# Kernel tuning notes

Measured on AMD Instinct MI355X. Metric: run time of the kernel, lower is better.

The kernel has to match this reference:

```python
import jax, jax.numpy as jnp
import numpy as np

DEPTH = 3
MAX_NB = 10
HIDDEN = 128


def setup_inputs() -> dict:
    key = jax.random.key(0)
    k = jax.random.split(key, 14)
    B, A, E, H, NB = 64, 1024, 2048, HIDDEN, MAX_NB
    s = 0.05
    return {
        "input_atom": jax.random.normal(k[0], (B, A, 82), jnp.float32),
        "input_bond": jax.random.normal(k[1], (B, E, 6), jnp.float32),
        "atom_graph": jax.random.randint(k[2], (B, A, NB), 0, A),
        "bond_graph": jax.random.randint(k[3], (B, A, NB), 0, E),
        "num_nbs": jax.random.randint(k[4], (B, A), 0, NB + 1),
        "node_mask": jnp.ones((B, A), jnp.float32),
        "W_atom": jax.random.normal(k[5], (82, H), jnp.float32) * s,
        "W_nei_atom": jax.random.normal(k[6], (H, H), jnp.float32) * s,
        "W_nei_bond": jax.random.normal(k[7], (6, H), jnp.float32) * s,
        "W_self": jax.random.normal(k[8], (H, H), jnp.float32) * s,
        "W_U2": jax.random.normal(k[9], (H + 6, H), jnp.float32) * s,
        "b_U2": jax.random.normal(k[10], (H,), jnp.float32) * s,
        "W_U1": jax.random.normal(k[11], (2 * H, H), jnp.float32) * s,
        "b_U1": jax.random.normal(k[12], (H,), jnp.float32) * s,
    }


def reference(input_atom, input_bond, atom_graph, bond_graph, num_nbs, node_mask,
              W_atom, W_nei_atom, W_nei_bond, W_self, W_U2, b_U2, W_U1, b_U1):
    B, A, NB = atom_graph.shape
    H = W_atom.shape[1]
    atom_features = input_atom @ W_atom                       # [B, A, H]
    # neighbor validity mask: [B, A, NB, 1]
    mask_nei = (jnp.arange(NB)[None, None, :] < num_nbs[:, :, None]).astype(jnp.float32)[..., None]
    idx_a = atom_graph.reshape(B, A * NB, 1)
    idx_b = bond_graph.reshape(B, A * NB, 1)
    # bond neighbor features are loop-invariant: gather once
    fbond_nei = jnp.take_along_axis(input_bond, idx_b, axis=1).reshape(B, A, NB, 6)
    h_nei_bond = fbond_nei @ W_nei_bond                       # [B, A, NB, H]
    node_m = node_mask[..., None]                             # [B, A, 1]
    kernel = None
    for _ in range(DEPTH):
        fatom_nei = jnp.take_along_axis(atom_features, idx_a, axis=1).reshape(B, A, NB, H)
        h_nei = (fatom_nei @ W_nei_atom) * h_nei_bond         # [B, A, NB, H]
        f_nei = jnp.sum(h_nei * mask_nei, axis=2)             # [B, A, H]
        f_self = atom_features @ W_self                        # [B, A, H]
        kernel = f_nei * f_self * node_m
        l_nei = jnp.concatenate([fatom_nei, fbond_nei], axis=3)  # [B, A, NB, H+6]
        pre_label = l_nei @ W_U2 + b_U2
        nei_label = jnp.sum(pre_label * mask_nei, axis=2)      # [B, A, H]
        new_label = jnp.concatenate([atom_features, nei_label], axis=2)
        atom_features = new_label @ W_U1 + b_U1
    return kernel, atom_features
```

## Files before the change

kernel.cpp:

```cpp
#include <hip/hip_runtime.h>

constexpr int NB = 10, H = 128;
constexpr int M = 64 * 1024;
constexpr long SL = (long)M * H;

typedef __attribute__((ext_vector_type(8))) short s16x8;
typedef __attribute__((ext_vector_type(4))) float f32x4;

__device__ __forceinline__ ushort f2b(float f) {
    union { float f; uint u; } v; v.f = f;
    uint u = v.u;
    uint r = u + 0x7fffu + ((u >> 16) & 1u);
    return (ushort)(r >> 16);
}
__device__ __forceinline__ float b2f(ushort u) {
    union { uint u; float f; } v; v.u = ((uint)u) << 16; return v.f;
}

__device__ __forceinline__ int swz(int bid, int cpx) {
    return (bid & 7) * cpx + (bid >> 3);
}

template<int NC, int FLAGS>
__device__ __forceinline__ void gemm_body(
    int tg, const ushort* __restrict__ Abf, const ushort* __restrict__ WT,
    const ushort* __restrict__ FNb, const float* __restrict__ nmask,
    float* __restrict__ Cf, ushort* __restrict__ Cb)
{
    constexpr bool KOUT = FLAGS & 8, OF32 = FLAGS & 16;
    constexpr int K = NC * 32;
    const int lane = threadIdx.x & 63, wid = threadIdx.x >> 6;
    const int l15 = lane & 15, g = lane >> 4;

    s16x8 w[2][NC];
    #pragma unroll
    for (int ct = 0; ct < 2; ++ct)
        #pragma unroll
        for (int kc = 0; kc < NC; ++kc)
            w[ct][kc] = *(const s16x8*)(WT + (size_t)((2 * wid + ct) * 16 + l15) * K + kc * 32 + g * 8);

    #pragma unroll
    for (int i = 0; i < 4; ++i) {
        const int m0 = (tg * 4 + i) * 16;
        s16x8 ac[NC];
        #pragma unroll
        for (int kc = 0; kc < NC; ++kc)
            ac[kc] = *(const s16x8*)(Abf + (size_t)(m0 + l15) * K + kc * 32 + g * 8);

        f32x4 acc[2];
        #pragma unroll
        for (int ct = 0; ct < 2; ++ct) acc[ct] = (f32x4){0.f, 0.f, 0.f, 0.f};
        #pragma unroll
        for (int kc = 0; kc < NC; ++kc)
            #pragma unroll
            for (int ct = 0; ct < 2; ++ct)
                acc[ct] = __builtin_amdgcn_mfma_f32_16x16x32_bf16(ac[kc], w[ct][kc], acc[ct], 0, 0, 0);

        #pragma unroll
        for (int ct = 0; ct < 2; ++ct) {
            const int col = (2 * wid + ct) * 16 + l15;
            #pragma unroll
            for (int r = 0; r < 4; ++r) {
                const int m = m0 + 4 * g + r;
                const size_t o = (size_t)m * H + col;
                float v = acc[ct][r];
                if constexpr (KOUT) v = v * b2f(FNb[o]) * nmask[m];
                if constexpr (OF32) Cf[o] = v; else Cb[o] = f2b(v);
            }
        }
    }
}

template<bool OF32>
__device__ __forceinline__ void u1f_body(
    int tg, const ushort* __restrict__ AF, const ushort* __restrict__ SATOM,
    const ushort* __restrict__ FBSb, const ushort* __restrict__ WT,
    float* __restrict__ Cf, ushort* __restrict__ Cb)
{
    const int lane = threadIdx.x & 63, wid = threadIdx.x >> 6;
    const int l15 = lane & 15, g = lane >> 4;

    s16x8 w[2][9];
    #pragma unroll
    for (int ct = 0; ct < 2; ++ct)
        #pragma unroll
        for (int kc = 0; kc < 9; ++kc)
            w[ct][kc] = *(const s16x8*)(WT + (size_t)((2 * wid + ct) * 16 + l15) * 288 + kc * 32 + g * 8);

    #pragma unroll
    for (int i = 0; i < 4; ++i) {
        const int m0 = (tg * 4 + i) * 16;
        const size_t rb = (size_t)(m0 + l15) * H + g * 8;
        s16x8 ac[9];
        #pragma unroll
        for (int kc = 0; kc < 4; ++kc) {
            ac[kc]     = *(const s16x8*)(AF    + rb + kc * 32);
            ac[kc + 4] = *(const s16x8*)(SATOM + rb + kc * 32);
        }
        ac[8] = (s16x8){0,0,0,0,0,0,0,0};
        if (g == 0) ac[8] = *(const s16x8*)(FBSb + (size_t)(m0 + l15) * 8);

        f32x4 acc[2];
        #pragma unroll
        for (int ct = 0; ct < 2; ++ct) acc[ct] = (f32x4){0.f, 0.f, 0.f, 0.f};
        #pragma unroll
        for (int kc = 0; kc < 9; ++kc)
            #pragma unroll
            for (int ct = 0; ct < 2; ++ct)
                acc[ct] = __builtin_amdgcn_mfma_f32_16x16x32_bf16(ac[kc], w[ct][kc], acc[ct], 0, 0, 0);

        #pragma unroll
        for (int ct = 0; ct < 2; ++ct) {
            const int col = (2 * wid + ct) * 16 + l15;
            #pragma unroll
            for (int r = 0; r < 4; ++r) {
                const size_t o = (size_t)(m0 + 4 * g + r) * H + col;
                if constexpr (OF32) Cf[o] = acc[ct][r]; else Cb[o] = f2b(acc[ct][r]);
            }
        }
    }
}

template<int NC, int FLAGS>
__global__ __launch_bounds__(256, 4) void gemm_af(
    const ushort* __restrict__ Abf, const ushort* __restrict__ WT,
    const ushort* __restrict__ FNb, const float* __restrict__ nmask,
    float* __restrict__ Cf, ushort* __restrict__ Cb)
{
    gemm_body<NC, FLAGS>(swz(blockIdx.x, 128), Abf, WT, FNb, nmask, Cf, Cb);
}

template<bool OF32>
__global__ __launch_bounds__(256, 4) void u1f(
    const ushort* __restrict__ AF, const ushort* __restrict__ SATOM,
    const ushort* __restrict__ FBSb, const ushort* __restrict__ WT,
    float* __restrict__ Cf, ushort* __restrict__ Cb)
{
    u1f_body<OF32>(swz(blockIdx.x, 128), AF, SATOM, FBSb, WT, Cf, Cb);
}

__global__ __launch_bounds__(256, 4) void final2(
    const ushort* __restrict__ AF, const ushort* __restrict__ SATl,
    const ushort* __restrict__ FBSb, const ushort* __restrict__ WTu1f,
    const ushort* __restrict__ WTslf, const ushort* __restrict__ FNEIb,
    const float* __restrict__ nmask, float* __restrict__ out1,
    float* __restrict__ out0)
{
    if (blockIdx.x < 1024)
        u1f_body<true>(swz(blockIdx.x, 128), AF, SATl, FBSb, WTu1f, out1, nullptr);
    else
        gemm_body<4, 8 | 16>(swz(blockIdx.x - 1024, 128), AF, WTslf, FNEIb,
                             nmask, out0, nullptr);
}

__global__ __launch_bounds__(256, 8) void gather_satom(
    const ushort* __restrict__ AF, const int* __restrict__ ag,
    const int* __restrict__ nn, ushort* __restrict__ SATOM)
{
    const int bid = swz(blockIdx.x, 512);
    const int m  = bid * 16 + (threadIdx.x >> 4);
    const int c8 = (threadIdx.x & 15) * 8;
    const int b  = m >> 10;
    const int nnb = nn[m];
    const ushort* AFb = AF + ((size_t)b << 10) * H + c8;
    const int* agm = ag + (size_t)m * NB;

    int2 iv0 = *(const int2*)(agm + 0);
    int2 iv1 = *(const int2*)(agm + 2);
    int2 iv2 = *(const int2*)(agm + 4);
    int2 iv3 = *(const int2*)(agm + 6);
    int2 iv4 = *(const int2*)(agm + 8);

    float sacc[8];
    #pragma unroll
    for (int i = 0; i < 8; ++i) sacc[i] = 0.f;

    #define GS_STEP(nb, ia)                                              \
    if ((nb) < nnb) {                                                    \
        s16x8 av = *(const s16x8*)(AFb + (size_t)(ia) * H);              \
        _Pragma("unroll")                                                \
        for (int i = 0; i < 8; ++i) sacc[i] += b2f((ushort)av[i]);       \
    }
    GS_STEP(0, iv0.x) GS_STEP(1, iv0.y)
    GS_STEP(2, iv1.x) GS_STEP(3, iv1.y)
    GS_STEP(4, iv2.x) GS_STEP(5, iv2.y)
    GS_STEP(6, iv3.x) GS_STEP(7, iv3.y)
    GS_STEP(8, iv4.x) GS_STEP(9, iv4.y)
    #undef GS_STEP

    s16x8 so;
    #pragma unroll
    for (int i = 0; i < 8; ++i) so[i] = (short)f2b(sacc[i]);
    *(s16x8*)(SATOM + (size_t)m * H + c8) = so;
}

__global__ __launch_bounds__(256, 4) void gather_last(
    const ushort* __restrict__ AF, const ushort* __restrict__ ATW,
    const ushort* __restrict__ HB, const int* __restrict__ ag,
    const int* __restrict__ bg, const int* __restrict__ nn,
    ushort* __restrict__ SATOM, ushort* __restrict__ FNEIb)
{
    const int bid = swz(blockIdx.x, 512);
    const int m  = bid * 16 + (threadIdx.x >> 4);
    const int c8 = (threadIdx.x & 15) * 8;
    const int b  = m >> 10;
    const int nnb = nn[m];
    const ushort* AFb  = AF  + ((size_t)b << 10) * H + c8;
    const ushort* ATWb = ATW + ((size_t)b << 10) * H + c8;
    const ushort* HBb  = HB  + ((size_t)b << 11) * H + c8;
    const int* agm = ag + (size_t)m * NB;
    const int* bgm = bg + (size_t)m * NB;

    int2 ia0 = *(const int2*)(agm + 0), ib0 = *(const int2*)(bgm + 0);
    int2 ia1 = *(const int2*)(agm + 2), ib1 = *(const int2*)(bgm + 2);
    int2 ia2 = *(const int2*)(agm + 4), ib2 = *(const int2*)(bgm + 4);
    int2 ia3 = *(const int2*)(agm + 6), ib3 = *(const int2*)(bgm + 6);
    int2 ia4 = *(const int2*)(agm + 8), ib4 = *(const int2*)(bgm + 8);

    float sacc[8], facc[8];
    #pragma unroll
    for (int i = 0; i < 8; ++i) { sacc[i] = 0.f; facc[i] = 0.f; }

    #define GL_STEP(nb, ia, ib)                                          \
    if ((nb) < nnb) {                                                    \
        s16x8 av = *(const s16x8*)(AFb  + (size_t)(ia) * H);             \
        s16x8 tv = *(const s16x8*)(ATWb + (size_t)(ia) * H);             \
        s16x8 hv = *(const s16x8*)(HBb  + (size_t)(ib) * H);             \
        _Pragma("unroll")                                                \
        for (int i = 0; i < 8; ++i) {                                    \
            sacc[i] += b2f((ushort)av[i]);                               \
            facc[i] += b2f((ushort)tv[i]) * b2f((ushort)hv[i]);          \
        }                                                                \
    }
    GL_STEP(0, ia0.x, ib0.x) GL_STEP(1, ia0.y, ib0.y)
    GL_STEP(2, ia1.x, ib1.x) GL_STEP(3, ia1.y, ib1.y)
    GL_STEP(4, ia2.x, ib2.x) GL_STEP(5, ia2.y, ib2.y)
    GL_STEP(6, ia3.x, ib3.x) GL_STEP(7, ia3.y, ib3.y)
    GL_STEP(8, ia4.x, ib4.x) GL_STEP(9, ia4.y, ib4.y)
    #undef GL_STEP

    s16x8 so, fo;
    #pragma unroll
    for (int i = 0; i < 8; ++i) { so[i] = (short)f2b(sacc[i]); fo[i] = (short)f2b(facc[i]); }
    *(s16x8*)(SATOM + (size_t)m * H + c8) = so;
    *(s16x8*)(FNEIb + (size_t)m * H + c8) = fo;
}

__global__ __launch_bounds__(256) void prep_all(
    const float* __restrict__ Wa, const float* __restrict__ Wna,
    const float* __restrict__ Ws, const float* __restrict__ Wu2,
    const float* __restrict__ bu2, const float* __restrict__ Wu1,
    const float* __restrict__ bu1, const float* __restrict__ bond,
    const int* __restrict__ bg, const int* __restrict__ nn,
    const float* __restrict__ ia, const float* __restrict__ Wnb,
    ushort* __restrict__ WTs, ushort* __restrict__ FBSb,
    ushort* __restrict__ AFin, ushort* __restrict__ HB)
{
    const int bid = blockIdx.x;
    if (bid < 320) {
        int t = bid * 256 + threadIdx.x;
        const int tid = t;
        if (t < 128 * 96) { int n = t / 96, k = t % 96;
            WTs[tid] = (k < 82) ? f2b(Wa[k * H + n]) : 0; return; }
        t -= 128 * 96;
        if (t < 128 * 128) { int n = t / 128, k = t % 128;
            WTs[tid] = f2b(Wna[k * H + n]); return; }
        t -= 128 * 128;
        if (t < 128 * 128) { int n = t / 128, k = t % 128;
            WTs[tid] = f2b(Ws[k * H + n]); return; }
        t -= 128 * 128;
        {
            const int n = t / 288, k = t % 288;
            float v = 0.f;
            if (k < 128) {
                v = Wu1[k * H + n];
            } else if (k < 256) {
                const int kk = k - 128;
                float s = 0.f;
                for (int j = 0; j < 128; ++j) s += Wu2[kk * H + j] * Wu1[(128 + j) * H + n];
                v = s;
            } else {
                const int j = k - 256;
                if (j < 6) {
                    float s = 0.f;
                    for (int q = 0; q < 128; ++q) s += Wu2[(128 + j) * H + q] * Wu1[(128 + q) * H + n];
                    v = s;
                } else if (j == 6) {
                    float s = 0.f;
                    for (int q = 0; q < 128; ++q) s += bu2[q] * Wu1[(128 + q) * H + n];
                    v = s;
                } else if (j == 7) {
                    v = bu1[n];
                }
            }
            WTs[tid] = f2b(v);
            return;
        }
    } else if (bid < 576) {
        const int m = (bid - 320) * 256 + threadIdx.x;
        const int b = m >> 10;
        const int nnb = nn[m];
        float s[6] = {0,0,0,0,0,0};
        for (int nb = 0; nb < nnb; ++nb) {
            const int ib = bg[m * NB + nb];
            const float* fb = bond + ((size_t)(b << 11) + (size_t)ib) * 6;
            #pragma unroll
            for (int j = 0; j < 6; ++j) s[j] += fb[j];
        }
        s16x8 o;
        #pragma unroll
        for (int j = 0; j < 6; ++j) o[j] = (short)f2b(s[j]);
        o[6] = (short)f2b((float)nnb);
        o[7] = (short)f2b(1.0f);
        *(s16x8*)(FBSb + (size_t)m * 8) = o;
    } else if (bid < 3648) {
        const int tid = (bid - 576) * 256 + threadIdx.x;
        const int m = tid / 12, c = (tid % 12) * 8;
        s16x8 v;
        #pragma unroll
        for (int i = 0; i < 8; ++i) {
            const int k = c + i;
            v[i] = (short)(k < 82 ? f2b(ia[(size_t)m * 82 + k]) : 0);
        }
        *(s16x8*)(AFin + (size_t)m * 96 + c) = v;
    } else {
        const int t = (bid - 3648) * 256 + threadIdx.x;
        const int r = t >> 4, c8 = (t & 15) * 8;
        const float* fb = bond + (size_t)r * 6;
        const float2 f01 = *(const float2*)fb;
        const float2 f23 = *(const float2*)(fb + 2);
        const float2 f45 = *(const float2*)(fb + 4);
        s16x8 o;
        #pragma unroll
        for (int i = 0; i < 8; ++i) {
            const int c = c8 + i;
            const float v = f01.x * Wnb[0 * H + c] + f01.y * Wnb[1 * H + c]
                          + f23.x * Wnb[2 * H + c] + f23.y * Wnb[3 * H + c]
                          + f45.x * Wnb[4 * H + c] + f45.y * Wnb[5 * H + c];
            o[i] = (short)f2b(v);
        }
        *(s16x8*)(HB + (size_t)r * H + c8) = o;
    }
}

extern "C" void kernel_launch(void* const* d_in, const int* in_sizes, int n_in,
                              void* d_out, int out_size, void* d_ws, size_t ws_size,
                              hipStream_t stream)
{
    (void)in_sizes; (void)n_in; (void)out_size; (void)ws_size;

    const float* input_atom = (const float*)d_in[0];
    const float* input_bond = (const float*)d_in[1];
    const int*   atom_graph = (const int*)d_in[2];
    const int*   bond_graph = (const int*)d_in[3];
    const int*   num_nbs    = (const int*)d_in[4];
    const float* node_mask  = (const float*)d_in[5];
    const float* W_atom     = (const float*)d_in[6];
    const float* W_nei_atom = (const float*)d_in[7];
    const float* W_nei_bond = (const float*)d_in[8];
    const float* W_self     = (const float*)d_in[9];
    const float* W_U2       = (const float*)d_in[10];
    const float* b_U2       = (const float*)d_in[11];
    const float* W_U1       = (const float*)d_in[12];
    const float* b_U1       = (const float*)d_in[13];

    char* ws = (char*)d_ws;
    const size_t MB = 1024 * 1024;
    ushort* AF0   = (ushort*)(ws);
    ushort* AF1   = (ushort*)(ws + 16 * MB);
    ushort* SATw  = (ushort*)(ws + 32 * MB);
    ushort* ATW   = SATw;
    ushort* AFin  = (ushort*)(ws + 48 * MB);
    ushort* HB    = (ushort*)(ws + 64 * MB);
    ushort* SATl  = (ushort*)(ws + 96 * MB);
    ushort* FBSb  = (ushort*)(ws + 112 * MB);
    ushort* WTs_  = (ushort*)(ws + 113 * MB);

    ushort* WTa   = WTs_;
    ushort* WTna  = WTa   + 128 * 96;
    ushort* WTslf = WTna  + 128 * 128;
    ushort* WTu1f = WTslf + 128 * 128;

    float*  out0  = (float*)d_out;
    float*  out1  = out0 + SL;
    ushort* FNEIb = AF1;

    prep_all<<<11840, 256, 0, stream>>>(W_atom, W_nei_atom, W_self, W_U2, b_U2,
                                        W_U1, b_U1, input_bond, bond_graph,
                                        num_nbs, input_atom, W_nei_bond,
                                        WTs_, FBSb, AFin, HB);

    gemm_af<3, 0><<<1024, 256, 0, stream>>>(AFin, WTa, nullptr, nullptr,
                                            nullptr, AF0);

    gather_satom<<<4096, 256, 0, stream>>>(AF0, atom_graph, num_nbs, SATw);
    u1f<false><<<1024, 256, 0, stream>>>(AF0, SATw, FBSb, WTu1f, nullptr, AF1);
    gather_satom<<<4096, 256, 0, stream>>>(AF1, atom_graph, num_nbs, SATw);
    u1f<false><<<1024, 256, 0, stream>>>(AF1, SATw, FBSb, WTu1f, nullptr, AF0);

    gemm_af<4, 0><<<1024, 256, 0, stream>>>(AF0, WTna, nullptr, nullptr,
                                            nullptr, ATW);
    gather_last<<<4096, 256, 0, stream>>>(AF0, ATW, HB, atom_graph, bond_graph,
                                          num_nbs, SATl, FNEIb);
    final2<<<2048, 256, 0, stream>>>(AF0, SATl, FBSb, WTu1f, WTslf, FNEIb,
                                     node_mask, out1, out0);
}
```

Before: 193.3 us.

## Fuse neighbor-sum gather into U1 GEMM and move bond projection off prep

The neighbor-feature sum is now computed per wave directly in registers and fed straight into the U1 MFMA GEMM, removing the separate gather_satom kernels and the SATOM round trip through memory. Each wave now owns 16 rows across all 128 output columns and reloads weights from global/L2 per MFMA instead of keeping them in registers. The bond-hidden projection HB moves from prep_all into the ATW GEMM launch so it can overlap with it, and gather_last no longer sums atom features. The cost is heavier per-wave register use and repeated weight loads, with fewer waves working on each gather.

```diff
diff --git a/kernel.cpp b/kernel.cpp
--- a/kernel.cpp
+++ b/kernel.cpp
@@ -72,140 +72,158 @@
 }
 
 template<bool OF32>
-__device__ __forceinline__ void u1f_body(
-    int tg, const ushort* __restrict__ AF, const ushort* __restrict__ SATOM,
-    const ushort* __restrict__ FBSb, const ushort* __restrict__ WT,
-    float* __restrict__ Cf, ushort* __restrict__ Cb)
-{
-    const int lane = threadIdx.x & 63, wid = threadIdx.x >> 6;
+__device__ __forceinline__ void gu1_body(
+    int t, const ushort* __restrict__ AF, const ushort* __restrict__ FBSb,
+    const ushort* __restrict__ WT, const int* __restrict__ ag,
+    const int* __restrict__ nn, float* __restrict__ Cf, ushort* __restrict__ Cb)
+{
+    const int lane = threadIdx.x & 63;
     const int l15 = lane & 15, g = lane >> 4;
-
-    s16x8 w[2][9];
-    #pragma unroll
-    for (int ct = 0; ct < 2; ++ct)
-        #pragma unroll
-        for (int kc = 0; kc < 9; ++kc)
-            w[ct][kc] = *(const s16x8*)(WT + (size_t)((2 * wid + ct) * 16 + l15) * 288 + kc * 32 + g * 8);
-
-    #pragma unroll
-    for (int i = 0; i < 4; ++i) {
-        const int m0 = (tg * 4 + i) * 16;
-        const size_t rb = (size_t)(m0 + l15) * H + g * 8;
-        s16x8 ac[9];
-        #pragma unroll
-        for (int kc = 0; kc < 4; ++kc) {
-            ac[kc]     = *(const s16x8*)(AF    + rb + kc * 32);
-            ac[kc + 4] = *(const s16x8*)(SATOM + rb + kc * 32);
-        }
-        ac[8] = (s16x8){0,0,0,0,0,0,0,0};
-        if (g == 0) ac[8] = *(const s16x8*)(FBSb + (size_t)(m0 + l15) * 8);
-
-        f32x4 acc[2];
-        #pragma unroll
-        for (int ct = 0; ct < 2; ++ct) acc[ct] = (f32x4){0.f, 0.f, 0.f, 0.f};
-        #pragma unroll
-        for (int kc = 0; kc < 9; ++kc)
-            #pragma unroll
-            for (int ct = 0; ct < 2; ++ct)
-                acc[ct] = __builtin_amdgcn_mfma_f32_16x16x32_bf16(ac[kc], w[ct][kc], acc[ct], 0, 0, 0);
-
-        #pragma unroll
-        for (int ct = 0; ct < 2; ++ct) {
-            const int col = (2 * wid + ct) * 16 + l15;
-            #pragma unroll
-            for (int r = 0; r < 4; ++r) {
-                const size_t o = (size_t)(m0 + 4 * g + r) * H + col;
-                if constexpr (OF32) Cf[o] = acc[ct][r]; else Cb[o] = f2b(acc[ct][r]);
-            }
-        }
-    }
-}
-
-template<int NC, int FLAGS>
-__global__ __launch_bounds__(256, 4) void gemm_af(
+    const int m0 = t * 16;
+    const int row = m0 + l15;
+    const int b = row >> 10;
+    const ushort* AFb = AF + ((size_t)b << 10) * H + g * 8;
+    const int* agm = ag + (size_t)row * NB;
+    const int nnb = nn[row];
+
+    int2 iv0 = *(const int2*)(agm + 0);
+    int2 iv1 = *(const int2*)(agm + 2);
+    int2 iv2 = *(const int2*)(agm + 4);
+    int2 iv3 = *(const int2*)(agm + 6);
+    int2 iv4 = *(const int2*)(agm + 8);
+
+    float sacc[4][8];
+    #pragma unroll
+    for (int kc = 0; kc < 4; ++kc)
+        #pragma unroll
+        for (int i = 0; i < 8; ++i) sacc[kc][i] = 0.f;
+
+    #define GU_STEP(nb, ia)                                               \
+    if ((nb) < nnb) {                                                     \
+        const ushort* src = AFb + (size_t)(ia) * H;                       \
+        _Pragma("unroll")                                                 \
+        for (int kc = 0; kc < 4; ++kc) {                                  \
+            s16x8 v = *(const s16x8*)(src + kc * 32);                     \
+            _Pragma("unroll")                                             \
+            for (int i = 0; i < 8; ++i) sacc[kc][i] += b2f((ushort)v[i]); \
+        }                                                                 \
+    }
+    GU_STEP(0, iv0.x) GU_STEP(1, iv0.y)
+    GU_STEP(2, iv1.x) GU_STEP(3, iv1.y)
+    GU_STEP(4, iv2.x) GU_STEP(5, iv2.y)
+    GU_STEP(6, iv3.x) GU_STEP(7, iv3.y)
+    GU_STEP(8, iv4.x) GU_STEP(9, iv4.y)
+    #undef GU_STEP
+
+    s16x8 pa[4];
+    #pragma unroll
+    for (int kc = 0; kc < 4; ++kc)
+        #pragma unroll
+        for (int i = 0; i < 8; ++i) pa[kc][i] = (short)f2b(sacc[kc][i]);
+
+    s16x8 af[4];
+    const size_t rb = (size_t)row * H + g * 8;
+    #pragma unroll
+    for (int kc = 0; kc < 4; ++kc)
+        af[kc] = *(const s16x8*)(AF + rb + kc * 32);
+    s16x8 fb8 = (s16x8){0,0,0,0,0,0,0,0};
+    if (g == 0) fb8 = *(const s16x8*)(FBSb + (size_t)row * 8);
+
+    f32x4 acc[8];
+    #pragma unroll
+    for (int c = 0; c < 8; ++c) acc[c] = (f32x4){0.f, 0.f, 0.f, 0.f};
+
+    #pragma unroll
+    for (int kc = 0; kc < 9; ++kc) {
+        const s16x8 a = (kc < 4) ? af[kc] : ((kc < 8) ? pa[kc - 4] : fb8);
+        #pragma unroll
+        for (int c = 0; c < 8; ++c) {
+            s16x8 w = *(const s16x8*)(WT + (size_t)(c * 16 + l15) * 288 + kc * 32 + g * 8);
+            acc[c] = __builtin_amdgcn_mfma_f32_16x16x32_bf16(a, w, acc[c], 0, 0, 0);
+        }
+    }
+
+    #pragma unroll
+    for (int c = 0; c < 8; ++c) {
+        const int col = c * 16 + l15;
+        #pragma unroll
+        for (int r = 0; r < 4; ++r) {
+            const size_t o = (size_t)(m0 + 4 * g + r) * H + col;
+            if constexpr (OF32) Cf[o] = acc[c][r]; else Cb[o] = f2b(acc[c][r]);
+        }
+    }
+}
+
+__global__ __launch_bounds__(256, 4) void fused_gu1(
+    const ushort* __restrict__ AF, const ushort* __restrict__ FBSb,
+    const ushort* __restrict__ WT, const int* __restrict__ ag,
+    const int* __restrict__ nn, ushort* __restrict__ Cb)
+{
+    const int t = swz(blockIdx.x, 128) * 4 + (threadIdx.x >> 6);
+    gu1_body<false>(t, AF, FBSb, WT, ag, nn, nullptr, Cb);
+}
+
+__global__ __launch_bounds__(256, 4) void gemm_af3(
     const ushort* __restrict__ Abf, const ushort* __restrict__ WT,
-    const ushort* __restrict__ FNb, const float* __restrict__ nmask,
-    float* __restrict__ Cf, ushort* __restrict__ Cb)
-{
-    gemm_body<NC, FLAGS>(swz(blockIdx.x, 128), Abf, WT, FNb, nmask, Cf, Cb);
-}
-
-template<bool OF32>
-__global__ __launch_bounds__(256, 4) void u1f(
-    const ushort* __restrict__ AF, const ushort* __restrict__ SATOM,
-    const ushort* __restrict__ FBSb, const ushort* __restrict__ WT,
-    float* __restrict__ Cf, ushort* __restrict__ Cb)
-{
-    u1f_body<OF32>(swz(blockIdx.x, 128), AF, SATOM, FBSb, WT, Cf, Cb);
+    ushort* __restrict__ Cb)
+{
+    gemm_body<3, 0>(swz(blockIdx.x, 128), Abf, WT, nullptr, nullptr, nullptr, Cb);
+}
+
+__global__ __launch_bounds__(256, 4) void gemm_atw_hb(
+    const ushort* __restrict__ AF, const ushort* __restrict__ WTna,
+    const float* __restrict__ bond, const float* __restrict__ Wnb,
+    ushort* __restrict__ ATW, ushort* __restrict__ HB)
+{
+    if (blockIdx.x < 1024) {
+        gemm_body<4, 0>(swz(blockIdx.x, 128), AF, WTna, nullptr, nullptr,
+                        nullptr, ATW);
+    } else {
+        const int t = (blockIdx.x - 1024) * 256 + threadIdx.x;
+        const int r = t >> 4, c8 = (t & 15) * 8;
+        const float* fb = bond + (size_t)r * 6;
+        const float2 f01 = *(const float2*)fb;
+        const float2 f23 = *(const float2*)(fb + 2);
+        const float2 f45 = *(const float2*)(fb + 4);
+        s16x8 o;
+        #pragma unroll
+        for (int i = 0; i < 8; ++i) {
+            const int c = c8 + i;
+            const float v = f01.x * Wnb[0 * H + c] + f01.y * Wnb[1 * H + c]
+                          + f23.x * Wnb[2 * H + c] + f23.y * Wnb[3 * H + c]
+                          + f45.x * Wnb[4 * H + c] + f45.y * Wnb[5 * H + c];
+            o[i] = (short)f2b(v);
+        }
+        *(s16x8*)(HB + (size_t)r * H + c8) = o;
+    }
 }
 
 __global__ __launch_bounds__(256, 4) void final2(
-    const ushort* __restrict__ AF, const ushort* __restrict__ SATl,
-    const ushort* __restrict__ FBSb, const ushort* __restrict__ WTu1f,
-    const ushort* __restrict__ WTslf, const ushort* __restrict__ FNEIb,
-    const float* __restrict__ nmask, float* __restrict__ out1,
-    float* __restrict__ out0)
-{
-    if (blockIdx.x < 1024)
-        u1f_body<true>(swz(blockIdx.x, 128), AF, SATl, FBSb, WTu1f, out1, nullptr);
-    else
+    const ushort* __restrict__ AF, const ushort* __restrict__ FBSb,
+    const ushort* __restrict__ WTu1f, const ushort* __restrict__ WTslf,
+    const ushort* __restrict__ FNEIb, const int* __restrict__ ag,
+    const int* __restrict__ nn, const float* __restrict__ nmask,
+    float* __restrict__ out1, float* __restrict__ out0)
+{
+    if (blockIdx.x < 1024) {
+        const int t = swz(blockIdx.x, 128) * 4 + (threadIdx.x >> 6);
+        gu1_body<true>(t, AF, FBSb, WTu1f, ag, nn, out1, nullptr);
+    } else {
         gemm_body<4, 8 | 16>(swz(blockIdx.x - 1024, 128), AF, WTslf, FNEIb,
                              nmask, out0, nullptr);
-}
-
-__global__ __launch_bounds__(256, 8) void gather_satom(
-    const ushort* __restrict__ AF, const int* __restrict__ ag,
-    const int* __restrict__ nn, ushort* __restrict__ SATOM)
+    }
+}
+
+__global__ __launch_bounds__(256, 8) void gather_fnei(
+    const ushort* __restrict__ ATW, const ushort* __restrict__ HB,
+    const int* __restrict__ ag, const int* __restrict__ bg,
+    const int* __restrict__ nn, ushort* __restrict__ FNEIb)
 {
     const int bid = swz(blockIdx.x, 512);
     const int m  = bid * 16 + (threadIdx.x >> 4);
     const int c8 = (threadIdx.x & 15) * 8;
     const int b  = m >> 10;
     const int nnb = nn[m];
-    const ushort* AFb = AF + ((size_t)b << 10) * H + c8;
-    const int* agm = ag + (size_t)m * NB;
-
-    int2 iv0 = *(const int2*)(agm + 0);
-    int2 iv1 = *(const int2*)(agm + 2);
-    int2 iv2 = *(const int2*)(agm + 4);
-    int2 iv3 = *(const int2*)(agm + 6);
-    int2 iv4 = *(const int2*)(agm + 8);
-
-    float sacc[8];
-    #pragma unroll
-    for (int i = 0; i < 8; ++i) sacc[i] = 0.f;
-
-    #define GS_STEP(nb, ia)                                              \
-    if ((nb) < nnb) {                                                    \
-        s16x8 av = *(const s16x8*)(AFb + (size_t)(ia) * H);              \
-        _Pragma("unroll")                                                \
-        for (int i = 0; i < 8; ++i) sacc[i] += b2f((ushort)av[i]);       \
-    }
-    GS_STEP(0, iv0.x) GS_STEP(1, iv0.y)
-    GS_STEP(2, iv1.x) GS_STEP(3, iv1.y)
-    GS_STEP(4, iv2.x) GS_STEP(5, iv2.y)
-    GS_STEP(6, iv3.x) GS_STEP(7, iv3.y)
-    GS_STEP(8, iv4.x) GS_STEP(9, iv4.y)
-    #undef GS_STEP
-
-    s16x8 so;
-    #pragma unroll
-    for (int i = 0; i < 8; ++i) so[i] = (short)f2b(sacc[i]);
-    *(s16x8*)(SATOM + (size_t)m * H + c8) = so;
-}
-
-__global__ __launch_bounds__(256, 4) void gather_last(
-    const ushort* __restrict__ AF, const ushort* __restrict__ ATW,
-    const ushort* __restrict__ HB, const int* __restrict__ ag,
-    const int* __restrict__ bg, const int* __restrict__ nn,
-    ushort* __restrict__ SATOM, ushort* __restrict__ FNEIb)
-{
-    const int bid = swz(blockIdx.x, 512);
-    const int m  = bid * 16 + (threadIdx.x >> 4);
-    const int c8 = (threadIdx.x & 15) * 8;
-    const int b  = m >> 10;
-    const int nnb = nn[m];
-    const ushort* AFb  = AF  + ((size_t)b << 10) * H + c8;
     const ushort* ATWb = ATW + ((size_t)b << 10) * H + c8;
     const ushort* HBb  = HB  + ((size_t)b << 11) * H + c8;
     const int* agm = ag + (size_t)m * NB;
@@ -217,32 +235,28 @@
     int2 ia3 = *(const int2*)(agm + 6), ib3 = *(const int2*)(bgm + 6);
     int2 ia4 = *(const int2*)(agm + 8), ib4 = *(const int2*)(bgm + 8);
 
-    float sacc[8], facc[8];
-    #pragma unroll
-    for (int i = 0; i < 8; ++i) { sacc[i] = 0.f; facc[i] = 0.f; }
-
-    #define GL_STEP(nb, ia, ib)                                          \
-    if ((nb) < nnb) {                                                    \
-        s16x8 av = *(const s16x8*)(AFb  + (size_t)(ia) * H);             \
-        s16x8 tv = *(const s16x8*)(ATWb + (size_t)(ia) * H);             \
-        s16x8 hv = *(const s16x8*)(HBb  + (size_t)(ib) * H);             \
-        _Pragma("unroll")                                                \
-        for (int i = 0; i < 8; ++i) {                                    \
-            sacc[i] += b2f((ushort)av[i]);                               \
-            facc[i] += b2f((ushort)tv[i]) * b2f((ushort)hv[i]);          \
-        }                                                                \
-    }
-    GL_STEP(0, ia0.x, ib0.x) GL_STEP(1, ia0.y, ib0.y)
-    GL_STEP(2, ia1.x, ib1.x) GL_STEP(3, ia1.y, ib1.y)
-    GL_STEP(4, ia2.x, ib2.x) GL_STEP(5, ia2.y, ib2.y)
-    GL_STEP(6, ia3.x, ib3.x) GL_STEP(7, ia3.y, ib3.y)
-    GL_STEP(8, ia4.x, ib4.x) GL_STEP(9, ia4.y, ib4.y)
-    #undef GL_STEP
-
-    s16x8 so, fo;
-    #pragma unroll
-    for (int i = 0; i < 8; ++i) { so[i] = (short)f2b(sacc[i]); fo[i] = (short)f2b(facc[i]); }
-    *(s16x8*)(SATOM + (size_t)m * H + c8) = so;
+    float facc[8];
+    #pragma unroll
+    for (int i = 0; i < 8; ++i) facc[i] = 0.f;
+
+    #define GF_STEP(nb, ia, ib)                                           \
+    if ((nb) < nnb) {                                                     \
+        s16x8 tv = *(const s16x8*)(ATWb + (size_t)(ia) * H);              \
+        s16x8 hv = *(const s16x8*)(HBb  + (size_t)(ib) * H);              \
+        _Pragma("unroll")                                                 \
+        for (int i = 0; i < 8; ++i)                                       \
+            facc[i] += b2f((ushort)tv[i]) * b2f((ushort)hv[i]);           \
+    }
+    GF_STEP(0, ia0.x, ib0.x) GF_STEP(1, ia0.y, ib0.y)
+    GF_STEP(2, ia1.x, ib1.x) GF_STEP(3, ia1.y, ib1.y)
+    GF_STEP(4, ia2.x, ib2.x) GF_STEP(5, ia2.y, ib2.y)
+    GF_STEP(6, ia3.x, ib3.x) GF_STEP(7, ia3.y, ib3.y)
+    GF_STEP(8, ia4.x, ib4.x) GF_STEP(9, ia4.y, ib4.y)
+    #undef GF_STEP
+
+    s16x8 fo;
+    #pragma unroll
+    for (int i = 0; i < 8; ++i) fo[i] = (short)f2b(facc[i]);
     *(s16x8*)(FNEIb + (size_t)m * H + c8) = fo;
 }
 
@@ -252,9 +266,9 @@
     const float* __restrict__ bu2, const float* __restrict__ Wu1,
     const float* __restrict__ bu1, const float* __restrict__ bond,
     const int* __restrict__ bg, const int* __restrict__ nn,
-    const float* __restrict__ ia, const float* __restrict__ Wnb,
+    const float* __restrict__ ia,
     ushort* __restrict__ WTs, ushort* __restrict__ FBSb,
-    ushort* __restrict__ AFin, ushort* __restrict__ HB)
+    ushort* __restrict__ AFin)
 {
     const int bid = blockIdx.x;
     if (bid < 320) {
@@ -313,7 +327,7 @@
         o[6] = (short)f2b((float)nnb);
         o[7] = (short)f2b(1.0f);
         *(s16x8*)(FBSb + (size_t)m * 8) = o;
-    } else if (bid < 3648) {
+    } else {
         const int tid = (bid - 576) * 256 + threadIdx.x;
         const int m = tid / 12, c = (tid % 12) * 8;
         s16x8 v;
@@ -323,23 +337,6 @@
             v[i] = (short)(k < 82 ? f2b(ia[(size_t)m * 82 + k]) : 0);
         }
         *(s16x8*)(AFin + (size_t)m * 96 + c) = v;
-    } else {
-        const int t = (bid - 3648) * 256 + threadIdx.x;
-        const int r = t >> 4, c8 = (t & 15) * 8;
-        const float* fb = bond + (size_t)r * 6;
-        const float2 f01 = *(const float2*)fb;
-        const float2 f23 = *(const float2*)(fb + 2);
-        const float2 f45 = *(const float2*)(fb + 4);
-        s16x8 o;
-        #pragma unroll
-        for (int i = 0; i < 8; ++i) {
-            const int c = c8 + i;
-            const float v = f01.x * Wnb[0 * H + c] + f01.y * Wnb[1 * H + c]
-                          + f23.x * Wnb[2 * H + c] + f23.y * Wnb[3 * H + c]
-                          + f45.x * Wnb[4 * H + c] + f45.y * Wnb[5 * H + c];
-            o[i] = (short)f2b(v);
-        }
-        *(s16x8*)(HB + (size_t)r * H + c8) = o;
     }
 }
 
@@ -368,11 +365,9 @@
     const size_t MB = 1024 * 1024;
     ushort* AF0   = (ushort*)(ws);
     ushort* AF1   = (ushort*)(ws + 16 * MB);
-    ushort* SATw  = (ushort*)(ws + 32 * MB);
-    ushort* ATW   = SATw;
+    ushort* ATW   = (ushort*)(ws + 32 * MB);
     ushort* AFin  = (ushort*)(ws + 48 * MB);
     ushort* HB    = (ushort*)(ws + 64 * MB);
-    ushort* SATl  = (ushort*)(ws + 96 * MB);
     ushort* FBSb  = (ushort*)(ws + 112 * MB);
     ushort* WTs_  = (ushort*)(ws + 113 * MB);
 
@@ -385,23 +380,16 @@
     float*  out1  = out0 + SL;
     ushort* FNEIb = AF1;
 
-    prep_all<<<11840, 256, 0, stream>>>(W_atom, W_nei_atom, W_self, W_U2, b_U2,
-                                        W_U1, b_U1, input_bond, bond_graph,
-                                        num_nbs, input_atom, W_nei_bond,
-                                        WTs_, FBSb, AFin, HB);
-
-    gemm_af<3, 0><<<1024, 256, 0, stream>>>(AFin, WTa, nullptr, nullptr,
-                                            nullptr, AF0);
-
-    gather_satom<<<4096, 256, 0, stream>>>(AF0, atom_graph, num_nbs, SATw);
-    u1f<false><<<1024, 256, 0, stream>>>(AF0, SATw, FBSb, WTu1f, nullptr, AF1);
-    gather_satom<<<4096, 256, 0, stream>>>(AF1, atom_graph, num_nbs, SATw);
-    u1f<false><<<1024, 256, 0, stream>>>(AF1, SATw, FBSb, WTu1f, nullptr, AF0);
-
-    gemm_af<4, 0><<<1024, 256, 0, stream>>>(AF0, WTna, nullptr, nullptr,
-                                            nullptr, ATW);
-    gather_last<<<4096, 256, 0, stream>>>(AF0, ATW, HB, atom_graph, bond_graph,
-                                          num_nbs, SATl, FNEIb);
-    final2<<<2048, 256, 0, stream>>>(AF0, SATl, FBSb, WTu1f, WTslf, FNEIb,
-                                     node_mask, out1, out0);
-}
+    prep_all<<<3648, 256, 0, stream>>>(W_atom, W_nei_atom, W_self, W_U2, b_U2,
+                                       W_U1, b_U1, input_bond, bond_graph,
+                                       num_nbs, input_atom, WTs_, FBSb, AFin);
+    gemm_af3<<<1024, 256, 0, stream>>>(AFin, WTa, AF0);
+    fused_gu1<<<1024, 256, 0, stream>>>(AF0, FBSb, WTu1f, atom_graph, num_nbs, AF1);
+    fused_gu1<<<1024, 256, 0, stream>>>(AF1, FBSb, WTu1f, atom_graph, num_nbs, AF0);
+    gemm_atw_hb<<<9216, 256, 0, stream>>>(AF0, WTna, input_bond, W_nei_bond,
+                                          ATW, HB);
+    gather_fnei<<<4096, 256, 0, stream>>>(ATW, HB, atom_graph, bond_graph,
+                                          num_nbs, FNEIb);
+    final2<<<2048, 256, 0, stream>>>(AF0, FBSb, WTu1f, WTslf, FNEIb,
+                                     atom_graph, num_nbs, node_mask, out1, out0);
+}
```

Measured after the change: 198.7 us. 1.03x slower.

## Fuse input-atom bf16 conversion and W_atom GEMM into prep kernel

Applied to the files above, without the earlier changes.

Replaces the separate conversion pass to a padded bf16 AFin buffer and the subsequent gemm_af launch with a fused MFMA body inside the prep kernel. It reads fp32 input_atom rows directly, converts them in registers, and multiplies by register-held W_atom fragments. This removes one kernel launch and the write and re-read of the intermediate buffer. The cost is scattered 2-byte output stores, unaligned float2 loads from 82-wide rows, and per-block recomputation of W_atom fragments.

```diff
diff --git a/kernel.cpp b/kernel.cpp
--- a/kernel.cpp
+++ b/kernel.cpp
@@ -246,23 +246,79 @@
     *(s16x8*)(FNEIb + (size_t)m * H + c8) = fo;
 }
 
-__global__ __launch_bounds__(256) void prep_all(
-    const float* __restrict__ Wa, const float* __restrict__ Wna,
-    const float* __restrict__ Ws, const float* __restrict__ Wu2,
-    const float* __restrict__ bu2, const float* __restrict__ Wu1,
-    const float* __restrict__ bu1, const float* __restrict__ bond,
-    const int* __restrict__ bg, const int* __restrict__ nn,
-    const float* __restrict__ ia, const float* __restrict__ Wnb,
-    ushort* __restrict__ WTs, ushort* __restrict__ FBSb,
-    ushort* __restrict__ AFin, ushort* __restrict__ HB)
+__device__ __forceinline__ void fa_body(
+    int tg, const float* __restrict__ ia, const float* __restrict__ Wa,
+    ushort* __restrict__ Cb)
+{
+    const int lane = threadIdx.x & 63, wid = threadIdx.x >> 6;
+    const int l15 = lane & 15, g = lane >> 4;
+
+    s16x8 w[2][3];
+    #pragma unroll
+    for (int ct = 0; ct < 2; ++ct) {
+        const int n = (2 * wid + ct) * 16 + l15;
+        #pragma unroll
+        for (int kc = 0; kc < 3; ++kc) {
+            s16x8 wv;
+            #pragma unroll
+            for (int i = 0; i < 8; ++i) {
+                const int k = kc * 32 + g * 8 + i;
+                wv[i] = (short)(k < 82 ? f2b(Wa[k * H + n]) : 0);
+            }
+            w[ct][kc] = wv;
+        }
+    }
+
+    #pragma unroll
+    for (int t = 0; t < 4; ++t) {
+        const int m0 = (tg * 4 + t) * 16;
+        const float* row = ia + (size_t)(m0 + l15) * 82;
+        s16x8 a[3];
+        #pragma unroll
+        for (int kc = 0; kc < 3; ++kc) {
+            #pragma unroll
+            for (int p = 0; p < 4; ++p) {
+                const int k = kc * 32 + g * 8 + 2 * p;
+                float2 v = (k < 82) ? *(const float2*)(row + k)
+                                    : make_float2(0.f, 0.f);
+                a[kc][2 * p]     = (short)f2b(v.x);
+                a[kc][2 * p + 1] = (short)f2b(v.y);
+            }
+        }
+        f32x4 acc[2];
+        #pragma unroll
+        for (int ct = 0; ct < 2; ++ct) acc[ct] = (f32x4){0.f, 0.f, 0.f, 0.f};
+        #pragma unroll
+        for (int kc = 0; kc < 3; ++kc)
+            #pragma unroll
+            for (int ct = 0; ct < 2; ++ct)
+                acc[ct] = __builtin_amdgcn_mfma_f32_16x16x32_bf16(a[kc], w[ct][kc], acc[ct], 0, 0, 0);
+        #pragma unroll
+        for (int ct = 0; ct < 2; ++ct) {
+            const int col = (2 * wid + ct) * 16 + l15;
+            #pragma unroll
+            for (int r = 0; r < 4; ++r)
+                Cb[(size_t)(m0 + 4 * g + r) * H + col] = f2b(acc[ct][r]);
+        }
+    }
+}
+
+__global__ __launch_bounds__(256, 4) void k0_prep_fa(
+    const float* __restrict__ ia, const float* __restrict__ Wa,
+    const float* __restrict__ Wna, const float* __restrict__ Ws,
+    const float* __restrict__ Wu2, const float* __restrict__ bu2,
+    const float* __restrict__ Wu1, const float* __restrict__ bu1,
+    const float* __restrict__ bond, const int* __restrict__ bg,
+    const int* __restrict__ nn, const float* __restrict__ Wnb,
+    ushort* __restrict__ AF0, ushort* __restrict__ WTs,
+    ushort* __restrict__ FBSb, ushort* __restrict__ HB)
 {
     const int bid = blockIdx.x;
-    if (bid < 320) {
-        int t = bid * 256 + threadIdx.x;
+    if (bid < 1024) {
+        fa_body(swz(bid, 128), ia, Wa, AF0);
+    } else if (bid < 1296) {
+        int t = (bid - 1024) * 256 + threadIdx.x;
         const int tid = t;
-        if (t < 128 * 96) { int n = t / 96, k = t % 96;
-            WTs[tid] = (k < 82) ? f2b(Wa[k * H + n]) : 0; return; }
-        t -= 128 * 96;
         if (t < 128 * 128) { int n = t / 128, k = t % 128;
             WTs[tid] = f2b(Wna[k * H + n]); return; }
         t -= 128 * 128;
@@ -296,8 +352,8 @@
             WTs[tid] = f2b(v);
             return;
         }
-    } else if (bid < 576) {
-        const int m = (bid - 320) * 256 + threadIdx.x;
+    } else if (bid < 1552) {
+        const int m = (bid - 1296) * 256 + threadIdx.x;
         const int b = m >> 10;
         const int nnb = nn[m];
         float s[6] = {0,0,0,0,0,0};
@@ -313,18 +369,8 @@
         o[6] = (short)f2b((float)nnb);
         o[7] = (short)f2b(1.0f);
         *(s16x8*)(FBSb + (size_t)m * 8) = o;
-    } else if (bid < 3648) {
-        const int tid = (bid - 576) * 256 + threadIdx.x;
-        const int m = tid / 12, c = (tid % 12) * 8;
-        s16x8 v;
-        #pragma unroll
-        for (int i = 0; i < 8; ++i) {
-            const int k = c + i;
-            v[i] = (short)(k < 82 ? f2b(ia[(size_t)m * 82 + k]) : 0);
-        }
-        *(s16x8*)(AFin + (size_t)m * 96 + c) = v;
     } else {
-        const int t = (bid - 3648) * 256 + threadIdx.x;
+        const int t = (bid - 1552) * 256 + threadIdx.x;
         const int r = t >> 4, c8 = (t & 15) * 8;
         const float* fb = bond + (size_t)r * 6;
         const float2 f01 = *(const float2*)fb;
@@ -370,14 +416,12 @@
     ushort* AF1   = (ushort*)(ws + 16 * MB);
     ushort* SATw  = (ushort*)(ws + 32 * MB);
     ushort* ATW   = SATw;
-    ushort* AFin  = (ushort*)(ws + 48 * MB);
     ushort* HB    = (ushort*)(ws + 64 * MB);
     ushort* SATl  = (ushort*)(ws + 96 * MB);
     ushort* FBSb  = (ushort*)(ws + 112 * MB);
     ushort* WTs_  = (ushort*)(ws + 113 * MB);
 
-    ushort* WTa   = WTs_;
-    ushort* WTna  = WTa   + 128 * 96;
+    ushort* WTna  = WTs_;
     ushort* WTslf = WTna  + 128 * 128;
     ushort* WTu1f = WTslf + 128 * 128;
 
@@ -385,13 +429,10 @@
     float*  out1  = out0 + SL;
     ushort* FNEIb = AF1;
 
-    prep_all<<<11840, 256, 0, stream>>>(W_atom, W_nei_atom, W_self, W_U2, b_U2,
-                                        W_U1, b_U1, input_bond, bond_graph,
-                                        num_nbs, input_atom, W_nei_bond,
-                                        WTs_, FBSb, AFin, HB);
-
-    gemm_af<3, 0><<<1024, 256, 0, stream>>>(AFin, WTa, nullptr, nullptr,
-                                            nullptr, AF0);
+    k0_prep_fa<<<9744, 256, 0, stream>>>(input_atom, W_atom, W_nei_atom,
+                                         W_self, W_U2, b_U2, W_U1, b_U1,
+                                         input_bond, bond_graph, num_nbs,
+                                         W_nei_bond, AF0, WTs_, FBSb, HB);
 
     gather_satom<<<4096, 256, 0, stream>>>(AF0, atom_graph, num_nbs, SATw);
     u1f<false><<<1024, 256, 0, stream>>>(AF0, SATw, FBSb, WTu1f, nullptr, AF1);
```

New measurement: 186.7 us. -3.4%, faster.
